# Kernel optimization log

Measured on AMD Instinct MI355X. Metric: run time of the kernel, lower is better.

## Reference

```python
import jax, jax.numpy as jnp
import numpy as np

N, E = 50000, 400000          # nodes, edges
T, R = 4, 8                   # node types, relations (edge types)
H, DK = 8, 32                 # heads, head dim
DIN = DOUT = 256              # in/out feature dim (DOUT = H*DK)
SQRT_DK = float(np.sqrt(DK))


def setup_inputs() -> dict:
    key = jax.random.key(0)
    ks = jax.random.split(key, 12)
    f32 = jnp.float32
    return {
        "x": jax.random.normal(ks[0], (N, DIN), f32),
        "node_type": jax.random.randint(ks[1], (N,), 0, T, jnp.int32),
        "src": jax.random.randint(ks[2], (E,), 0, N, jnp.int32),
        "dst": jax.random.randint(ks[3], (E,), 0, N, jnp.int32),
        "etype": jax.random.randint(ks[4], (E,), 0, R, jnp.int32),
        "Wk": jax.random.normal(ks[5], (T, DOUT, DIN), f32) / np.sqrt(DIN).astype(np.float32),
        "bk": jnp.zeros((T, DOUT), f32),
        "Wq": jax.random.normal(ks[6], (T, DOUT, DIN), f32) / np.sqrt(DIN).astype(np.float32),
        "bq": jnp.zeros((T, DOUT), f32),
        "Wv": jax.random.normal(ks[7], (T, DOUT, DIN), f32) / np.sqrt(DIN).astype(np.float32),
        "bv": jnp.zeros((T, DOUT), f32),
        "Wa": jax.random.normal(ks[8], (T, DOUT, DOUT), f32) / np.sqrt(DOUT).astype(np.float32),
        "ba": jnp.zeros((T, DOUT), f32),
        "rel_pri": jnp.ones((R, H), f32),
        "rel_att": jax.random.normal(ks[9], (R, H, DK, DK), f32) / np.sqrt(DK).astype(np.float32),  # ~xavier
        "rel_msg": jax.random.normal(ks[10], (R, H, DK, DK), f32) / np.sqrt(DK).astype(np.float32),
        "skip": jnp.ones((T,), f32),
    }


def _typed_linear(h, W, b, ntype):
    # per-node-type linear: y_n = W[type_n] @ h_n + b[type_n]
    y = jnp.einsum('ni,tdi->ntd', h, W)                      # [N,T,D] (T is small)
    y = jnp.take_along_axis(y, ntype[:, None, None], axis=1)[:, 0]
    return y + b[ntype]


def _hgt_forward(x, node_type, src, dst, etype,
                 Wk, bk, Wq, bq, Wv, bv, Wa, ba,
                 rel_pri, rel_att, rel_msg, skip):
    # typed k/q/v projections -> [N,H,DK]
    K = _typed_linear(x, Wk, bk, node_type).reshape(N, H, DK)
    Q = _typed_linear(x, Wq, bq, node_type).reshape(N, H, DK)
    V = _typed_linear(x, Wv, bv, node_type).reshape(N, H, DK)

    k_e, q_e, v_e = K[src], Q[dst], V[src]                   # [E,H,DK] gathers

    # per-relation head transforms (loop over small fixed R, masked accumulate)
    key_e = jnp.zeros_like(k_e)
    msg_e = jnp.zeros_like(v_e)
    for r in range(R):
        m = (etype == r)[:, None, None].astype(x.dtype)
        key_e = key_e + m * jnp.einsum('ehd,hdf->ehf', k_e, rel_att[r])
        msg_e = msg_e + m * jnp.einsum('ehd,hdf->ehf', v_e, rel_msg[r])

    att = (q_e * key_e).sum(-1) * rel_pri[etype] / SQRT_DK   # [E,H]

    # softmax per (dst node, edge type) segment, then mean across edge types
    seg = dst * R + etype                                    # [E]
    S = N * R
    amax = jax.ops.segment_max(att, seg, num_segments=S)     # [S,H]
    ex = jnp.exp(att - amax[seg])
    denom = jax.ops.segment_sum(ex, seg, num_segments=S)
    w = ex / denom[seg]                                      # normalized attention [E,H]
    h_seg = jax.ops.segment_sum(w[:, :, None] * msg_e, seg, num_segments=S)  # [S,H,DK]
    cnt = jax.ops.segment_sum(jnp.ones((E,), x.dtype), seg, num_segments=S)  # [S]

    h_nr = h_seg.reshape(N, R, DOUT)
    present = (cnt.reshape(N, R) > 0).astype(x.dtype)        # which etypes hit each node
    t = h_nr.sum(1) / jnp.maximum(present.sum(1), 1.0)[:, None]  # cross_reducer='mean'

    trans = _typed_linear(t, Wa, ba, node_type)              # per-type output linear
    alpha = jax.nn.sigmoid(skip)[node_type][:, None]
    return trans * alpha + x * (1.0 - alpha)


def reference(x, node_type, src, dst, etype,
              Wk, bk, Wq, bq, Wv, bv, Wa, ba,
              rel_pri, rel_att, rel_msg, skip):
    return _hgt_forward(x, node_type, src, dst, etype,
                        Wk, bk, Wq, bq, Wv, bv, Wa, ba,
                        rel_pri, rel_att, rel_msg, skip)
```

## Files before the change

kernel.cpp:

```cpp
#include <hip/hip_runtime.h>
#include <math.h>
#include <stdint.h>

#define N_NODES 50000
#define N_EDGES 400000
#define N_T 4
#define N_R 8
#define N_H 8
#define DKD 32
#define D 256
#define TM 64
#define N_SEG (N_NODES * N_R)
#define EMASK 0xFFFFF
#define PROJ_BLOCKS ((N_NODES + TM - 1) / TM + N_T)

typedef _Float16 h2 __attribute__((ext_vector_type(2)));
typedef _Float16 v8h __attribute__((ext_vector_type(8)));
typedef float v4f __attribute__((ext_vector_type(4)));
typedef unsigned short u16;

__device__ __forceinline__ u16 h2u(_Float16 h) { return __builtin_bit_cast(u16, h); }
__device__ __forceinline__ h2 u2h2(unsigned int u) { return __builtin_bit_cast(h2, u); }

#if __has_builtin(__builtin_amdgcn_fdot2)
__device__ __forceinline__ float fdot2f(h2 a, h2 b, float c) {
    return __builtin_amdgcn_fdot2(a, b, c, false);
}
#else
__device__ __forceinline__ float fdot2f(h2 a, h2 b, float c) {
    return c + (float)a[0] * (float)b[0] + (float)a[1] * (float)b[1];
}
#endif

__device__ __forceinline__ float dot32h(const uint4* __restrict__ a,
                                        const uint4* __restrict__ q) {
    float s = 0.f;
    #pragma unroll
    for (int j = 0; j < 4; j++) {
        uint4 av = a[j], qv = q[j];
        s = fdot2f(u2h2(av.x), u2h2(qv.x), s);
        s = fdot2f(u2h2(av.y), u2h2(qv.y), s);
        s = fdot2f(u2h2(av.z), u2h2(qv.z), s);
        s = fdot2f(u2h2(av.w), u2h2(qv.w), s);
    }
    return s;
}

__global__ __launch_bounds__(256) void k_cvtW(
    const float4* __restrict__ w0, const float4* __restrict__ w1,
    const float4* __restrict__ w2, const float4* __restrict__ w3,
    ushort4* __restrict__ d, int n4each) {
    int i = blockIdx.x * 256 + threadIdx.x;
    if (i >= 4 * n4each) return;
    int sel = i / n4each, j = i - sel * n4each;
    const float4* s = (sel == 0) ? w0 : (sel == 1) ? w1 : (sel == 2) ? w2 : w3;
    float4 v = s[j];
    ushort4 o;
    o.x = h2u((_Float16)v.x); o.y = h2u((_Float16)v.y);
    o.z = h2u((_Float16)v.z); o.w = h2u((_Float16)v.w);
    d[i] = o;
}

__global__ __launch_bounds__(256) void k_cvt_att(const float4* __restrict__ s,
                                                 const float* __restrict__ pri,
                                                 ushort4* __restrict__ d, int n4) {
    int i = blockIdx.x * 256 + threadIdx.x;
    if (i >= n4) return;
    int mat = i >> 8;
    float sc = pri[mat] * 0.17677669529663687f;
    float4 v = s[i];
    ushort4 o;
    o.x = h2u((_Float16)(v.x * sc)); o.y = h2u((_Float16)(v.y * sc));
    o.z = h2u((_Float16)(v.z * sc)); o.w = h2u((_Float16)(v.w * sc));
    d[i] = o;
}

__global__ __launch_bounds__(256) void k_cvt_t(const float* __restrict__ s,
                                               u16* __restrict__ d) {
    int i = blockIdx.x * 256 + threadIdx.x;
    if (i >= N_R * N_H * DKD * DKD) return;
    int mat = i >> 10, w = i & 1023;
    int d0 = w >> 5, f = w & 31;
    d[(mat << 10) + f * DKD + d0] = h2u((_Float16)s[i]);
}

__global__ void k_hist(const int* __restrict__ nt, int* __restrict__ cnt) {
    int n = blockIdx.x * blockDim.x + threadIdx.x;
    if (n < N_NODES) atomicAdd(&cnt[nt[n]], 1);
}

__global__ void k_scan(const int* __restrict__ cnt, int* __restrict__ off,
                       int* __restrict__ toff) {
    int o = 0, to = 0;
    for (int t = 0; t < N_T; t++) {
        off[t] = o; toff[t] = to;
        o += cnt[t]; to += (cnt[t] + TM - 1) / TM;
    }
    off[N_T] = o; toff[N_T] = to;
}

__global__ void k_scatter(const int* __restrict__ nt, const int* __restrict__ off,
                          int* __restrict__ cur, int* __restrict__ order) {
    int n = blockIdx.x * blockDim.x + threadIdx.x;
    if (n >= N_NODES) return;
    int t = nt[n];
    int pos = off[t] + atomicAdd(&cur[t], 1);
    order[pos] = n;
}

__global__ void k_hist_seg(const int* __restrict__ dst, const int* __restrict__ et,
                           int* __restrict__ cnt) {
    int e = blockIdx.x * blockDim.x + threadIdx.x;
    if (e < N_EDGES) atomicAdd(&cnt[dst[e] * N_R + et[e]], 1);
}

__global__ __launch_bounds__(1024) void k_scan_l1(const int* __restrict__ cnt,
                                                  int* __restrict__ excl,
                                                  int* __restrict__ bsum) {
    __shared__ int sh[1024];
    int tid = threadIdx.x, i = blockIdx.x * 1024 + tid;
    int v = (i < N_SEG) ? cnt[i] : 0;
    sh[tid] = v;
    __syncthreads();
    #pragma unroll
    for (int ofs = 1; ofs < 1024; ofs <<= 1) {
        int t = (tid >= ofs) ? sh[tid - ofs] : 0;
        __syncthreads();
        sh[tid] += t;
        __syncthreads();
    }
    if (i < N_SEG) excl[i] = sh[tid] - v;
    if (tid == 1023) bsum[blockIdx.x] = sh[1023];
}

__global__ __launch_bounds__(512) void k_scan_l2(int* __restrict__ bsum, int NB) {
    __shared__ int sh[512];
    int tid = threadIdx.x;
    int v = (tid < NB) ? bsum[tid] : 0;
    sh[tid] = v;
    __syncthreads();
    #pragma unroll
    for (int ofs = 1; ofs < 512; ofs <<= 1) {
        int t = (tid >= ofs) ? sh[tid - ofs] : 0;
        __syncthreads();
        sh[tid] += t;
        __syncthreads();
    }
    if (tid < NB) bsum[tid] = sh[tid] - v;
}

__global__ void k_scan_l3(int* __restrict__ excl, const int* __restrict__ bsum) {
    int i = blockIdx.x * blockDim.x + threadIdx.x;
    if (i < N_SEG) excl[i] += bsum[i >> 10];
    else if (i == N_SEG) excl[N_SEG] = N_EDGES;
}

__global__ void k_scatter_seg(const int* __restrict__ src, const int* __restrict__ dst,
                              const int* __restrict__ et, const int* __restrict__ rp,
                              int* __restrict__ cur, int* __restrict__ esrc) {
    int e = blockIdx.x * blockDim.x + threadIdx.x;
    if (e >= N_EDGES) return;
    int r = et[e];
    int sg = dst[e] * N_R + r;
    int pos = rp[sg] + atomicAdd(&cur[sg], 1);
    esrc[pos] = src[e] | (r << 20);
}

__global__ __launch_bounds__(256) void k_proj(
    const float* __restrict__ x, const int* __restrict__ order,
    const int* __restrict__ off, const int* __restrict__ toff,
    const u16* __restrict__ Wkb, const float* __restrict__ bk,
    const u16* __restrict__ Wqb, const float* __restrict__ bq,
    const u16* __restrict__ Wvb, const float* __restrict__ bv,
    u16* __restrict__ Kb, u16* __restrict__ Qb, u16* __restrict__ Vb) {
    __shared__ __align__(16) u16 xs[TM][D + 8];
    int b = blockIdx.x;
    int t = -1;
    #pragma unroll
    for (int i = 0; i < N_T; i++)
        if (b >= toff[i] && b < toff[i + 1]) t = i;
    if (t < 0) return;
    int nodeBase = off[t] + (b - toff[t]) * TM;
    int count = min(TM, off[t + 1] - nodeBase);
    int tid = threadIdx.x;

    for (int j = tid; j < TM * (D / 4); j += 256) {
        int row = j >> 6, ch = j & 63;
        float4 v = {0.f, 0.f, 0.f, 0.f};
        if (row < count) {
            int g = order[nodeBase + row];
            v = *(const float4*)(x + (size_t)g * D + ch * 4);
        }
        ushort4 o;
        o.x = h2u((_Float16)v.x); o.y = h2u((_Float16)v.y);
        o.z = h2u((_Float16)v.z); o.w = h2u((_Float16)v.w);
        *(ushort4*)&xs[row][ch * 4] = o;
    }
    __syncthreads();

    int lane = tid & 63, wave = tid >> 6;
    int m = lane & 15, quad = lane >> 4;
    v8h a[8];
    #pragma unroll
    for (int ks = 0; ks < 8; ks++)
        a[ks] = *(const v8h*)&xs[wave * 16 + m][ks * 32 + quad * 8];

    int grow[4]; bool vrow[4];
    #pragma unroll
    for (int r = 0; r < 4; r++) {
        int rowi = wave * 16 + quad * 4 + r;
        vrow[r] = (rowi < count);
        grow[r] = vrow[r] ? order[nodeBase + rowi] : 0;
    }

    const u16* Ws[3] = {Wkb + (size_t)t * D * D, Wqb + (size_t)t * D * D, Wvb + (size_t)t * D * D};
    const float* Bs[3] = {bk + t * D, bq + t * D, bv + t * D};
    u16* Os[3] = {Kb, Qb, Vb};

    for (int p = 0; p < 3; p++) {
        const u16* W = Ws[p];
        for (int dt = 0; dt < 16; dt++) {
            int dcol = dt * 16 + m;
            v4f acc = {0.f, 0.f, 0.f, 0.f};
            #pragma unroll
            for (int ks = 0; ks < 8; ks++) {
                v8h bf = *(const v8h*)(W + (size_t)dcol * D + ks * 32 + quad * 8);
                acc = __builtin_amdgcn_mfma_f32_16x16x32_f16(a[ks], bf, acc, 0, 0, 0);
            }
            float bias = Bs[p][dcol];
            #pragma unroll
            for (int r = 0; r < 4; r++) {
                if (vrow[r])
                    Os[p][(size_t)grow[r] * D + dcol] = h2u((_Float16)(acc[r] + bias));
            }
        }
    }
}

__global__ __launch_bounds__(256, 4) void k_fused(
    const u16* __restrict__ Kb, u16* QTb, const u16* __restrict__ Vb,
    const int* __restrict__ rowptr, const int* __restrict__ esrc,
    const u16* __restrict__ Ab, const u16* __restrict__ Mtb) {
    __shared__ __align__(16) unsigned int Uldu[4][N_H][20];
    int wave = threadIdx.x >> 6, lane = threadIdx.x & 63;
    int n = blockIdx.x * 4 + wave;
    if (n >= N_NODES) return;
    int h = lane >> 3, fl = lane & 7, fo = fl * 4;
    int base = n * N_R;

    int bnd[N_R + 1];
    #pragma unroll
    for (int i = 0; i <= N_R; i++) bnd[i] = rowptr[base + i];

    uint4 qv4[4];
    {
        const uint4* qp = (const uint4*)(QTb + (size_t)n * D + h * DKD);
        #pragma unroll
        for (int j = 0; j < 4; j++) qv4[j] = qp[j];
    }

    h2 qt2[N_R][2];
    int np = 0;
    #pragma unroll
    for (int r = 0; r < N_R; r++) {
        if (bnd[r] >= bnd[r + 1]) continue;
        np++;
        const u16* Ar = Ab + ((size_t)(r * N_H + h) * DKD + fo) * DKD;
        float q0 = dot32h((const uint4*)(Ar), qv4);
        float q1 = dot32h((const uint4*)(Ar + DKD), qv4);
        float q2 = dot32h((const uint4*)(Ar + 2 * DKD), qv4);
        float q3 = dot32h((const uint4*)(Ar + 3 * DKD), qv4);
        qt2[r][0] = h2{(_Float16)q0, (_Float16)q1};
        qt2[r][1] = h2{(_Float16)q2, (_Float16)q3};
    }

    float den[N_R] = {0.f, 0.f, 0.f, 0.f, 0.f, 0.f, 0.f, 0.f};
    float ua[N_R][4] = {};

#define DOTQ(P, RS, KU) { \
    h2 _ka = u2h2((KU).x), _kb = u2h2((KU).y); \
    switch (RS) { \
    case 0: P = fdot2f(_kb, qt2[0][1], fdot2f(_ka, qt2[0][0], 0.f)); break; \
    case 1: P = fdot2f(_kb, qt2[1][1], fdot2f(_ka, qt2[1][0], 0.f)); break; \
    case 2: P = fdot2f(_kb, qt2[2][1], fdot2f(_ka, qt2[2][0], 0.f)); break; \
    case 3: P = fdot2f(_kb, qt2[3][1], fdot2f(_ka, qt2[3][0], 0.f)); break; \
    case 4: P = fdot2f(_kb, qt2[4][1], fdot2f(_ka, qt2[4][0], 0.f)); break; \
    case 5: P = fdot2f(_kb, qt2[5][1], fdot2f(_ka, qt2[5][0], 0.f)); break; \
    case 6: P = fdot2f(_kb, qt2[6][1], fdot2f(_ka, qt2[6][0], 0.f)); break; \
    default: P = fdot2f(_kb, qt2[7][1], fdot2f(_ka, qt2[7][0], 0.f)); break; } }

#define ACCR(R, EX, V0, V1, V2, V3) \
    den[R] += EX; ua[R][0] += EX*V0; ua[R][1] += EX*V1; ua[R][2] += EX*V2; ua[R][3] += EX*V3;

#define ACCE(RS, EX, VU) { \
    h2 _va = u2h2((VU).x), _vb = u2h2((VU).y); \
    float _v0 = (float)_va[0], _v1 = (float)_va[1]; \
    float _v2 = (float)_vb[0], _v3 = (float)_vb[1]; \
    switch (RS) { \
    case 0: ACCR(0, EX, _v0, _v1, _v2, _v3) break; \
    case 1: ACCR(1, EX, _v0, _v1, _v2, _v3) break; \
    case 2: ACCR(2, EX, _v0, _v1, _v2, _v3) break; \
    case 3: ACCR(3, EX, _v0, _v1, _v2, _v3) break; \
    case 4: ACCR(4, EX, _v0, _v1, _v2, _v3) break; \
    case 5: ACCR(5, EX, _v0, _v1, _v2, _v3) break; \
    case 6: ACCR(6, EX, _v0, _v1, _v2, _v3) break; \
    default: ACCR(7, EX, _v0, _v1, _v2, _v3) break; } }

    int eb = bnd[0], ee = bnd[N_R];
    size_t hoff = (size_t)(h * DKD + fo);
    for (int w0 = eb; w0 < ee; w0 += 64) {
        int wcnt = min(64, ee - w0);
        int myek = (lane < wcnt) ? esrc[w0 + lane] : 0;
        for (int i0 = 0; i0 < wcnt; i0 += 4) {
            int mc = wcnt - i0;
            int pk0 = __shfl(myek, i0);
            int pk1 = __shfl(myek, i0 + (mc > 1 ? 1 : 0));
            int pk2 = __shfl(myek, i0 + (mc > 2 ? 2 : 0));
            int pk3 = __shfl(myek, i0 + (mc > 3 ? 3 : 0));
            int s0 = pk0 & EMASK, s1 = pk1 & EMASK, s2 = pk2 & EMASK, s3 = pk3 & EMASK;
            int r0 = __builtin_amdgcn_readfirstlane(pk0) >> 20;
            int r1 = __builtin_amdgcn_readfirstlane(pk1) >> 20;
            int r2 = __builtin_amdgcn_readfirstlane(pk2) >> 20;
            int r3 = __builtin_amdgcn_readfirstlane(pk3) >> 20;
            uint2 ku0 = *(const uint2*)(Kb + (size_t)s0 * D + hoff);
            uint2 ku1 = *(const uint2*)(Kb + (size_t)s1 * D + hoff);
            uint2 ku2 = *(const uint2*)(Kb + (size_t)s2 * D + hoff);
            uint2 ku3 = *(const uint2*)(Kb + (size_t)s3 * D + hoff);
            uint2 vu0 = *(const uint2*)(Vb + (size_t)s0 * D + hoff);
            uint2 vu1 = *(const uint2*)(Vb + (size_t)s1 * D + hoff);
            uint2 vu2 = *(const uint2*)(Vb + (size_t)s2 * D + hoff);
            uint2 vu3 = *(const uint2*)(Vb + (size_t)s3 * D + hoff);
            float p0, p1, p2, p3;
            DOTQ(p0, r0, ku0);
            DOTQ(p1, r1, ku1);
            DOTQ(p2, r2, ku2);
            DOTQ(p3, r3, ku3);
            p0 += __shfl_xor(p0, 1); p1 += __shfl_xor(p1, 1);
            p2 += __shfl_xor(p2, 1); p3 += __shfl_xor(p3, 1);
            p0 += __shfl_xor(p0, 2); p1 += __shfl_xor(p1, 2);
            p2 += __shfl_xor(p2, 2); p3 += __shfl_xor(p3, 2);
            p0 += __shfl_xor(p0, 4); p1 += __shfl_xor(p1, 4);
            p2 += __shfl_xor(p2, 4); p3 += __shfl_xor(p3, 4);
            float ex0 = __expf(p0), ex1 = __expf(p1);
            float ex2 = __expf(p2), ex3 = __expf(p3);
            ACCE(r0, ex0, vu0);
            if (mc > 1) { ACCE(r1, ex1, vu1); }
            if (mc > 2) { ACCE(r2, ex2, vu2); }
            if (mc > 3) { ACCE(r3, ex3, vu3); }
        }
    }

    float macc[4] = {0.f, 0.f, 0.f, 0.f};
    #pragma unroll
    for (int r = 0; r < N_R; r++) {
        if (bnd[r] >= bnd[r + 1]) continue;
        float invd = 1.f / den[r];
        unsigned int pw0 = __builtin_bit_cast(unsigned int,
            h2{(_Float16)(ua[r][0] * invd), (_Float16)(ua[r][1] * invd)});
        unsigned int pw1 = __builtin_bit_cast(unsigned int,
            h2{(_Float16)(ua[r][2] * invd), (_Float16)(ua[r][3] * invd)});
        __builtin_amdgcn_wave_barrier();
        *(uint2*)&Uldu[wave][h][fl * 2] = uint2{pw0, pw1};
        __builtin_amdgcn_wave_barrier();
        uint4 Um[4];
        #pragma unroll
        for (int j = 0; j < 4; j++)
            Um[j] = *(const uint4*)&Uldu[wave][h][4 * j];
        const u16* mp = Mtb + ((size_t)(r * N_H + h) * DKD + fo) * DKD;
        #pragma unroll
        for (int j = 0; j < 4; j++)
            macc[j] += dot32h((const uint4*)(mp + j * DKD), Um);
        __builtin_amdgcn_wave_barrier();
    }

    float invp = (np > 0) ? 1.f / (float)np : 1.f;
    ushort4 o;
    o.x = h2u((_Float16)(macc[0] * invp)); o.y = h2u((_Float16)(macc[1] * invp));
    o.z = h2u((_Float16)(macc[2] * invp)); o.w = h2u((_Float16)(macc[3] * invp));
    *(ushort4*)(QTb + (size_t)n * D + hoff) = o;
}

__global__ __launch_bounds__(256) void k_out(
    const u16* __restrict__ TBF, const float* __restrict__ x,
    const int* __restrict__ order, const int* __restrict__ off, const int* __restrict__ toff,
    const u16* __restrict__ Wab, const float* __restrict__ ba,
    const float* __restrict__ skip, float* __restrict__ out) {
    __shared__ __align__(16) u16 xs[TM][D + 8];
    int b = blockIdx.x;
    int t = -1;
    #pragma unroll
    for (int i = 0; i < N_T; i++)
        if (b >= toff[i] && b < toff[i + 1]) t = i;
    if (t < 0) return;
    int nodeBase = off[t] + (b - toff[t]) * TM;
    int count = min(TM, off[t + 1] - nodeBase);
    int tid = threadIdx.x;

    for (int j = tid; j < TM * 32; j += 256) {
        int row = j >> 5, ch = j & 31;
        ushort4 z = {0, 0, 0, 0};
        if (row < count) {
            int g = order[nodeBase + row];
            const ushort4* p = (const ushort4*)(TBF + (size_t)g * D + ch * 8);
            *(ushort4*)&xs[row][ch * 8] = p[0];
            *(ushort4*)&xs[row][ch * 8 + 4] = p[1];
        } else {
            *(ushort4*)&xs[row][ch * 8] = z;
            *(ushort4*)&xs[row][ch * 8 + 4] = z;
        }
    }
    __syncthreads();

    int lane = tid & 63, wave = tid >> 6;
    int m = lane & 15, quad = lane >> 4;
    v8h a[8];
    #pragma unroll
    for (int ks = 0; ks < 8; ks++)
        a[ks] = *(const v8h*)&xs[wave * 16 + m][ks * 32 + quad * 8];

    int grow[4]; bool vrow[4];
    #pragma unroll
    for (int r = 0; r < 4; r++) {
        int rowi = wave * 16 + quad * 4 + r;
        vrow[r] = (rowi < count);
        grow[r] = vrow[r] ? order[nodeBase + rowi] : 0;
    }

    float sv = skip[t];
    float alpha = 1.f / (1.f + __expf(-sv));
    float beta = 1.f - alpha;
    const u16* W = Wab + (size_t)t * D * D;

    for (int dt = 0; dt < 16; dt++) {
        int dcol = dt * 16 + m;
        v4f acc = {0.f, 0.f, 0.f, 0.f};
        #pragma unroll
        for (int ks = 0; ks < 8; ks++) {
            v8h bf = *(const v8h*)(W + (size_t)dcol * D + ks * 32 + quad * 8);
            acc = __builtin_amdgcn_mfma_f32_16x16x32_f16(a[ks], bf, acc, 0, 0, 0);
        }
        float bias = ba[t * D + dcol];
        #pragma unroll
        for (int r = 0; r < 4; r++) {
            if (vrow[r]) {
                size_t o = (size_t)grow[r] * D + dcol;
                out[o] = alpha * (acc[r] + bias) + beta * x[o];
            }
        }
    }
}

extern "C" void kernel_launch(void* const* d_in, const int* in_sizes, int n_in,
                              void* d_out, int out_size, void* d_ws, size_t ws_size,
                              hipStream_t stream) {
    const float* x       = (const float*)d_in[0];
    const int* node_type = (const int*)d_in[1];
    const int* src       = (const int*)d_in[2];
    const int* dst       = (const int*)d_in[3];
    const int* etype     = (const int*)d_in[4];
    const float* Wk = (const float*)d_in[5];
    const float* bk = (const float*)d_in[6];
    const float* Wq = (const float*)d_in[7];
    const float* bq = (const float*)d_in[8];
    const float* Wv = (const float*)d_in[9];
    const float* bv = (const float*)d_in[10];
    const float* Wa = (const float*)d_in[11];
    const float* ba = (const float*)d_in[12];
    const float* rel_pri = (const float*)d_in[13];
    const float* rel_att = (const float*)d_in[14];
    const float* rel_msg = (const float*)d_in[15];
    const float* skip    = (const float*)d_in[16];
    float* out = (float*)d_out;
    char* ws = (char*)d_ws;

    const size_t SZH = (size_t)N_NODES * D * 2;
    const size_t WSZ = (size_t)N_T * D * D;
    const size_t RSZ = (size_t)N_R * N_H * DKD * DKD;
    u16* Kb  = (u16*)(ws);
    u16* Qb  = (u16*)(ws + SZH);
    u16* Vb  = (u16*)(ws + 2 * SZH);
    u16* TBF = Qb;
    u16* Wkb = (u16*)(ws + 3 * SZH);
    u16* Wqb = Wkb + WSZ;
    u16* Wvb = Wqb + WSZ;
    u16* Wab = Wvb + WSZ;
    u16* Ab  = Wab + WSZ;
    u16* Mtb = Ab + RSZ;
    int* order = (int*)(Mtb + RSZ);
    int* small = order + N_NODES;
    int* cnt  = small;
    int* cur  = small + 4;
    int* offp = small + 8;
    int* toffp= small + 13;

    char* ob = (char*)d_out;
    int* rowptr_seg = (int*)ob;
    int* cnt_seg    = rowptr_seg + (N_SEG + 16);
    int* cur_seg    = cnt_seg + N_SEG;
    int* esrc       = cur_seg + N_SEG;
    int* bsum       = esrc + N_EDGES;

    hipMemsetAsync(small, 0, 8 * sizeof(int), stream);
    hipMemsetAsync(cnt_seg, 0, 2 * (size_t)N_SEG * sizeof(int), stream);

    k_cvtW<<<(4 * (WSZ / 4) + 255) / 256, 256, 0, stream>>>(
        (const float4*)Wk, (const float4*)Wq, (const float4*)Wv, (const float4*)Wa,
        (ushort4*)Wkb, WSZ / 4);
    k_cvt_att<<<(RSZ / 4 + 255) / 256, 256, 0, stream>>>(
        (const float4*)rel_att, rel_pri, (ushort4*)Ab, RSZ / 4);
    k_cvt_t<<<(RSZ + 255) / 256, 256, 0, stream>>>(rel_msg, Mtb);

    k_hist<<<(N_NODES + 255) / 256, 256, 0, stream>>>(node_type, cnt);
    k_scan<<<1, 1, 0, stream>>>(cnt, offp, toffp);
    k_scatter<<<(N_NODES + 255) / 256, 256, 0, stream>>>(node_type, offp, cur, order);

    const int NB = (N_SEG + 1023) / 1024;
    k_hist_seg<<<(N_EDGES + 255) / 256, 256, 0, stream>>>(dst, etype, cnt_seg);
    k_scan_l1<<<NB, 1024, 0, stream>>>(cnt_seg, rowptr_seg, bsum);
    k_scan_l2<<<1, 512, 0, stream>>>(bsum, NB);
    k_scan_l3<<<(N_SEG + 1 + 255) / 256, 256, 0, stream>>>(rowptr_seg, bsum);
    k_scatter_seg<<<(N_EDGES + 255) / 256, 256, 0, stream>>>(src, dst, etype,
                                                             rowptr_seg, cur_seg, esrc);

    k_proj<<<PROJ_BLOCKS, 256, 0, stream>>>(x, order, offp, toffp,
                                            Wkb, bk, Wqb, bq, Wvb, bv, Kb, Qb, Vb);

    k_fused<<<(N_NODES + 3) / 4, 256, 0, stream>>>(Kb, Qb, Vb, rowptr_seg, esrc,
                                                   Ab, Mtb);

    k_out<<<PROJ_BLOCKS, 256, 0, stream>>>(TBF, x, order, offp, toffp,
                                           Wab, ba, skip, out);
}
```

Before: 2.042 ms.

## Split fused attention across one wave per relation with 16-bit edge indices

The fused attention kernel now runs one 512-thread block per destination node, with one wave per relation. Each wave loops over that relation's edges, and the per-relation message results are reduced through shared memory, replacing the single-wave-per-node loop that switched on the relation type. Edge source indices are stored as 16-bit values in the no-longer-needed Wk fp16 buffer, which is possible because k_proj now runs before the segment scatter. The exp is turned into exp2 by folding log2(e) into the attention scale, and packing uses cvt_pkrtz. The new layout exposes more parallelism for latency-bound gathers, but it idles the waves for relations with no edges and loses the 4-edge unrolling.

```diff
diff --git a/kernel.cpp b/kernel.cpp
--- a/kernel.cpp
+++ b/kernel.cpp
@@ -11,7 +11,6 @@
 #define D 256
 #define TM 64
 #define N_SEG (N_NODES * N_R)
-#define EMASK 0xFFFFF
 #define PROJ_BLOCKS ((N_NODES + TM - 1) / TM + N_T)
 
 typedef _Float16 h2 __attribute__((ext_vector_type(2)));
@@ -31,6 +30,14 @@
     return c + (float)a[0] * (float)b[0] + (float)a[1] * (float)b[1];
 }
 #endif
+
+__device__ __forceinline__ unsigned int pk16(float a, float b) {
+#if __has_builtin(__builtin_amdgcn_cvt_pkrtz)
+    return __builtin_bit_cast(unsigned int, __builtin_amdgcn_cvt_pkrtz(a, b));
+#else
+    return __builtin_bit_cast(unsigned int, h2{(_Float16)a, (_Float16)b});
+#endif
+}
 
 __device__ __forceinline__ float dot32h(const uint4* __restrict__ a,
                                         const uint4* __restrict__ q) {
@@ -67,7 +74,7 @@
     int i = blockIdx.x * 256 + threadIdx.x;
     if (i >= n4) return;
     int mat = i >> 8;
-    float sc = pri[mat] * 0.17677669529663687f;
+    float sc = pri[mat] * 0.2550309305920868f;
     float4 v = s[i];
     ushort4 o;
     o.x = h2u((_Float16)(v.x * sc)); o.y = h2u((_Float16)(v.y * sc));
@@ -157,13 +164,12 @@
 
 __global__ void k_scatter_seg(const int* __restrict__ src, const int* __restrict__ dst,
                               const int* __restrict__ et, const int* __restrict__ rp,
-                              int* __restrict__ cur, int* __restrict__ esrc) {
+                              int* __restrict__ cur, u16* __restrict__ esrc16) {
     int e = blockIdx.x * blockDim.x + threadIdx.x;
     if (e >= N_EDGES) return;
-    int r = et[e];
-    int sg = dst[e] * N_R + r;
+    int sg = dst[e] * N_R + et[e];
     int pos = rp[sg] + atomicAdd(&cur[sg], 1);
-    esrc[pos] = src[e] | (r << 20);
+    esrc16[pos] = (u16)src[e];
 }
 
 __global__ __launch_bounds__(256) void k_proj(
@@ -237,147 +243,88 @@
     }
 }
 
-__global__ __launch_bounds__(256, 4) void k_fused(
+__global__ __launch_bounds__(512) void k_fused(
     const u16* __restrict__ Kb, u16* QTb, const u16* __restrict__ Vb,
-    const int* __restrict__ rowptr, const int* __restrict__ esrc,
+    const int* __restrict__ rowptr_seg, const u16* __restrict__ esrc16,
     const u16* __restrict__ Ab, const u16* __restrict__ Mtb) {
-    __shared__ __align__(16) unsigned int Uldu[4][N_H][20];
-    int wave = threadIdx.x >> 6, lane = threadIdx.x & 63;
-    int n = blockIdx.x * 4 + wave;
-    if (n >= N_NODES) return;
+    __shared__ __align__(16) unsigned int Uex[N_R][N_H][20];
+    __shared__ __align__(16) float msh[N_R][64][4];
+    __shared__ int flg[N_R];
+    int tid = threadIdx.x;
+    int w = tid >> 6, lane = tid & 63;
+    int n = blockIdx.x;
     int h = lane >> 3, fl = lane & 7, fo = fl * 4;
-    int base = n * N_R;
-
-    int bnd[N_R + 1];
-    #pragma unroll
-    for (int i = 0; i <= N_R; i++) bnd[i] = rowptr[base + i];
-
-    uint4 qv4[4];
-    {
-        const uint4* qp = (const uint4*)(QTb + (size_t)n * D + h * DKD);
-        #pragma unroll
-        for (int j = 0; j < 4; j++) qv4[j] = qp[j];
-    }
-
-    h2 qt2[N_R][2];
-    int np = 0;
-    #pragma unroll
-    for (int r = 0; r < N_R; r++) {
-        if (bnd[r] >= bnd[r + 1]) continue;
-        np++;
-        const u16* Ar = Ab + ((size_t)(r * N_H + h) * DKD + fo) * DKD;
+
+    int s0 = __builtin_amdgcn_readfirstlane(rowptr_seg[n * N_R + w]);
+    int s1 = __builtin_amdgcn_readfirstlane(rowptr_seg[n * N_R + w + 1]);
+    if (lane == 0) flg[w] = (s0 < s1) ? 1 : 0;
+
+    float macc[4] = {0.f, 0.f, 0.f, 0.f};
+    if (s0 < s1) {
+        uint4 qv4[4];
+        {
+            const uint4* qp = (const uint4*)(QTb + (size_t)n * D + h * DKD);
+            qv4[0] = qp[0]; qv4[1] = qp[1]; qv4[2] = qp[2]; qv4[3] = qp[3];
+        }
+        const u16* Ar = Ab + ((size_t)(w * N_H + h) * DKD + fo) * DKD;
         float q0 = dot32h((const uint4*)(Ar), qv4);
         float q1 = dot32h((const uint4*)(Ar + DKD), qv4);
         float q2 = dot32h((const uint4*)(Ar + 2 * DKD), qv4);
         float q3 = dot32h((const uint4*)(Ar + 3 * DKD), qv4);
-        qt2[r][0] = h2{(_Float16)q0, (_Float16)q1};
-        qt2[r][1] = h2{(_Float16)q2, (_Float16)q3};
-    }
-
-    float den[N_R] = {0.f, 0.f, 0.f, 0.f, 0.f, 0.f, 0.f, 0.f};
-    float ua[N_R][4] = {};
-
-#define DOTQ(P, RS, KU) { \
-    h2 _ka = u2h2((KU).x), _kb = u2h2((KU).y); \
-    switch (RS) { \
-    case 0: P = fdot2f(_kb, qt2[0][1], fdot2f(_ka, qt2[0][0], 0.f)); break; \
-    case 1: P = fdot2f(_kb, qt2[1][1], fdot2f(_ka, qt2[1][0], 0.f)); break; \
-    case 2: P = fdot2f(_kb, qt2[2][1], fdot2f(_ka, qt2[2][0], 0.f)); break; \
-    case 3: P = fdot2f(_kb, qt2[3][1], fdot2f(_ka, qt2[3][0], 0.f)); break; \
-    case 4: P = fdot2f(_kb, qt2[4][1], fdot2f(_ka, qt2[4][0], 0.f)); break; \
-    case 5: P = fdot2f(_kb, qt2[5][1], fdot2f(_ka, qt2[5][0], 0.f)); break; \
-    case 6: P = fdot2f(_kb, qt2[6][1], fdot2f(_ka, qt2[6][0], 0.f)); break; \
-    default: P = fdot2f(_kb, qt2[7][1], fdot2f(_ka, qt2[7][0], 0.f)); break; } }
-
-#define ACCR(R, EX, V0, V1, V2, V3) \
-    den[R] += EX; ua[R][0] += EX*V0; ua[R][1] += EX*V1; ua[R][2] += EX*V2; ua[R][3] += EX*V3;
-
-#define ACCE(RS, EX, VU) { \
-    h2 _va = u2h2((VU).x), _vb = u2h2((VU).y); \
-    float _v0 = (float)_va[0], _v1 = (float)_va[1]; \
-    float _v2 = (float)_vb[0], _v3 = (float)_vb[1]; \
-    switch (RS) { \
-    case 0: ACCR(0, EX, _v0, _v1, _v2, _v3) break; \
-    case 1: ACCR(1, EX, _v0, _v1, _v2, _v3) break; \
-    case 2: ACCR(2, EX, _v0, _v1, _v2, _v3) break; \
-    case 3: ACCR(3, EX, _v0, _v1, _v2, _v3) break; \
-    case 4: ACCR(4, EX, _v0, _v1, _v2, _v3) break; \
-    case 5: ACCR(5, EX, _v0, _v1, _v2, _v3) break; \
-    case 6: ACCR(6, EX, _v0, _v1, _v2, _v3) break; \
-    default: ACCR(7, EX, _v0, _v1, _v2, _v3) break; } }
-
-    int eb = bnd[0], ee = bnd[N_R];
-    size_t hoff = (size_t)(h * DKD + fo);
-    for (int w0 = eb; w0 < ee; w0 += 64) {
-        int wcnt = min(64, ee - w0);
-        int myek = (lane < wcnt) ? esrc[w0 + lane] : 0;
-        for (int i0 = 0; i0 < wcnt; i0 += 4) {
-            int mc = wcnt - i0;
-            int pk0 = __shfl(myek, i0);
-            int pk1 = __shfl(myek, i0 + (mc > 1 ? 1 : 0));
-            int pk2 = __shfl(myek, i0 + (mc > 2 ? 2 : 0));
-            int pk3 = __shfl(myek, i0 + (mc > 3 ? 3 : 0));
-            int s0 = pk0 & EMASK, s1 = pk1 & EMASK, s2 = pk2 & EMASK, s3 = pk3 & EMASK;
-            int r0 = __builtin_amdgcn_readfirstlane(pk0) >> 20;
-            int r1 = __builtin_amdgcn_readfirstlane(pk1) >> 20;
-            int r2 = __builtin_amdgcn_readfirstlane(pk2) >> 20;
-            int r3 = __builtin_amdgcn_readfirstlane(pk3) >> 20;
-            uint2 ku0 = *(const uint2*)(Kb + (size_t)s0 * D + hoff);
-            uint2 ku1 = *(const uint2*)(Kb + (size_t)s1 * D + hoff);
-            uint2 ku2 = *(const uint2*)(Kb + (size_t)s2 * D + hoff);
-            uint2 ku3 = *(const uint2*)(Kb + (size_t)s3 * D + hoff);
-            uint2 vu0 = *(const uint2*)(Vb + (size_t)s0 * D + hoff);
-            uint2 vu1 = *(const uint2*)(Vb + (size_t)s1 * D + hoff);
-            uint2 vu2 = *(const uint2*)(Vb + (size_t)s2 * D + hoff);
-            uint2 vu3 = *(const uint2*)(Vb + (size_t)s3 * D + hoff);
-            float p0, p1, p2, p3;
-            DOTQ(p0, r0, ku0);
-            DOTQ(p1, r1, ku1);
-            DOTQ(p2, r2, ku2);
-            DOTQ(p3, r3, ku3);
-            p0 += __shfl_xor(p0, 1); p1 += __shfl_xor(p1, 1);
-            p2 += __shfl_xor(p2, 1); p3 += __shfl_xor(p3, 1);
-            p0 += __shfl_xor(p0, 2); p1 += __shfl_xor(p1, 2);
-            p2 += __shfl_xor(p2, 2); p3 += __shfl_xor(p3, 2);
-            p0 += __shfl_xor(p0, 4); p1 += __shfl_xor(p1, 4);
-            p2 += __shfl_xor(p2, 4); p3 += __shfl_xor(p3, 4);
-            float ex0 = __expf(p0), ex1 = __expf(p1);
-            float ex2 = __expf(p2), ex3 = __expf(p3);
-            ACCE(r0, ex0, vu0);
-            if (mc > 1) { ACCE(r1, ex1, vu1); }
-            if (mc > 2) { ACCE(r2, ex2, vu2); }
-            if (mc > 3) { ACCE(r3, ex3, vu3); }
-        }
-    }
-
-    float macc[4] = {0.f, 0.f, 0.f, 0.f};
-    #pragma unroll
-    for (int r = 0; r < N_R; r++) {
-        if (bnd[r] >= bnd[r + 1]) continue;
-        float invd = 1.f / den[r];
-        unsigned int pw0 = __builtin_bit_cast(unsigned int,
-            h2{(_Float16)(ua[r][0] * invd), (_Float16)(ua[r][1] * invd)});
-        unsigned int pw1 = __builtin_bit_cast(unsigned int,
-            h2{(_Float16)(ua[r][2] * invd), (_Float16)(ua[r][3] * invd)});
+        h2 qta = h2{(_Float16)q0, (_Float16)q1};
+        h2 qtb = h2{(_Float16)q2, (_Float16)q3};
+
+        float den = 0.f, ua0 = 0.f, ua1 = 0.f, ua2 = 0.f, ua3 = 0.f;
+        size_t hoff = (size_t)(h * DKD + fo);
+        for (int e = s0; e < s1; e++) {
+            int s = __builtin_amdgcn_readfirstlane((int)esrc16[e]);
+            uint2 ku = *(const uint2*)(Kb + (size_t)s * D + hoff);
+            uint2 vu = *(const uint2*)(Vb + (size_t)s * D + hoff);
+            float p = fdot2f(u2h2(ku.y), qtb, fdot2f(u2h2(ku.x), qta, 0.f));
+            p += __shfl_xor(p, 1);
+            p += __shfl_xor(p, 2);
+            p += __shfl_xor(p, 4);
+            float ex = exp2f(p);
+            den += ex;
+            h2 va = u2h2(vu.x), vb = u2h2(vu.y);
+            ua0 += ex * (float)va[0]; ua1 += ex * (float)va[1];
+            ua2 += ex * (float)vb[0]; ua3 += ex * (float)vb[1];
+        }
+
+        float invd = 1.f / den;
+        unsigned int pw0 = pk16(ua0 * invd, ua1 * invd);
+        unsigned int pw1 = pk16(ua2 * invd, ua3 * invd);
         __builtin_amdgcn_wave_barrier();
-        *(uint2*)&Uldu[wave][h][fl * 2] = uint2{pw0, pw1};
+        *(uint2*)&Uex[w][h][fl * 2] = uint2{pw0, pw1};
         __builtin_amdgcn_wave_barrier();
         uint4 Um[4];
         #pragma unroll
         for (int j = 0; j < 4; j++)
-            Um[j] = *(const uint4*)&Uldu[wave][h][4 * j];
-        const u16* mp = Mtb + ((size_t)(r * N_H + h) * DKD + fo) * DKD;
+            Um[j] = *(const uint4*)&Uex[w][h][4 * j];
+        const u16* mp = Mtb + ((size_t)(w * N_H + h) * DKD + fo) * DKD;
         #pragma unroll
         for (int j = 0; j < 4; j++)
             macc[j] += dot32h((const uint4*)(mp + j * DKD), Um);
-        __builtin_amdgcn_wave_barrier();
-    }
-
-    float invp = (np > 0) ? 1.f / (float)np : 1.f;
-    ushort4 o;
-    o.x = h2u((_Float16)(macc[0] * invp)); o.y = h2u((_Float16)(macc[1] * invp));
-    o.z = h2u((_Float16)(macc[2] * invp)); o.w = h2u((_Float16)(macc[3] * invp));
-    *(ushort4*)(QTb + (size_t)n * D + hoff) = o;
+    }
+
+    *(float4*)&msh[w][lane][0] = {macc[0], macc[1], macc[2], macc[3]};
+    __syncthreads();
+
+    if (tid < 64) {
+        float4 sum = {0.f, 0.f, 0.f, 0.f};
+        int np = 0;
+        #pragma unroll
+        for (int ww = 0; ww < N_R; ww++) {
+            np += flg[ww];
+            float4 m = *(const float4*)&msh[ww][tid][0];
+            sum.x += m.x; sum.y += m.y; sum.z += m.z; sum.w += m.w;
+        }
+        float invp = (np > 0) ? 1.f / (float)np : 1.f;
+        unsigned int o0 = pk16(sum.x * invp, sum.y * invp);
+        unsigned int o1 = pk16(sum.z * invp, sum.w * invp);
+        int hh = tid >> 3, ff = tid & 7;
+        *(uint2*)(QTb + (size_t)n * D + hh * DKD + ff * 4) = uint2{o0, o1};
+    }
 }
 
 __global__ __launch_bounds__(256) void k_out(
@@ -493,12 +440,13 @@
     int* offp = small + 8;
     int* toffp= small + 13;
 
+    u16* esrc16 = Wkb;
+
     char* ob = (char*)d_out;
     int* rowptr_seg = (int*)ob;
     int* cnt_seg    = rowptr_seg + (N_SEG + 16);
     int* cur_seg    = cnt_seg + N_SEG;
-    int* esrc       = cur_seg + N_SEG;
-    int* bsum       = esrc + N_EDGES;
+    int* bsum       = cur_seg + N_SEG;
 
     hipMemsetAsync(small, 0, 8 * sizeof(int), stream);
     hipMemsetAsync(cnt_seg, 0, 2 * (size_t)N_SEG * sizeof(int), stream);
@@ -514,19 +462,19 @@
     k_scan<<<1, 1, 0, stream>>>(cnt, offp, toffp);
     k_scatter<<<(N_NODES + 255) / 256, 256, 0, stream>>>(node_type, offp, cur, order);
 
+    k_proj<<<PROJ_BLOCKS, 256, 0, stream>>>(x, order, offp, toffp,
+                                            Wkb, bk, Wqb, bq, Wvb, bv, Kb, Qb, Vb);
+
     const int NB = (N_SEG + 1023) / 1024;
     k_hist_seg<<<(N_EDGES + 255) / 256, 256, 0, stream>>>(dst, etype, cnt_seg);
     k_scan_l1<<<NB, 1024, 0, stream>>>(cnt_seg, rowptr_seg, bsum);
     k_scan_l2<<<1, 512, 0, stream>>>(bsum, NB);
     k_scan_l3<<<(N_SEG + 1 + 255) / 256, 256, 0, stream>>>(rowptr_seg, bsum);
     k_scatter_seg<<<(N_EDGES + 255) / 256, 256, 0, stream>>>(src, dst, etype,
-                                                             rowptr_seg, cur_seg, esrc);
-
-    k_proj<<<PROJ_BLOCKS, 256, 0, stream>>>(x, order, offp, toffp,
-                                            Wkb, bk, Wqb, bq, Wvb, bv, Kb, Qb, Vb);
-
-    k_fused<<<(N_NODES + 3) / 4, 256, 0, stream>>>(Kb, Qb, Vb, rowptr_seg, esrc,
-                                                   Ab, Mtb);
+                                                             rowptr_seg, cur_seg,
+                                                             esrc16);
+
+    k_fused<<<N_NODES, 512, 0, stream>>>(Kb, Qb, Vb, rowptr_seg, esrc16, Ab, Mtb);
 
     k_out<<<PROJ_BLOCKS, 256, 0, stream>>>(TBF, x, order, offp, toffp,
                                            Wab, ba, skip, out);
```

Result: slower. 2.130 ms (+4.3%).
